# Optimization experiments

Hardware: AMD Instinct MI355X
Metric: run time of the kernel (lower is better)

Reference implementation:

```python
import jax, jax.numpy as jnp
import numpy as np

B, C, H, W = 16, 256, 56, 56
CR = C // 4
PAD = 1
NUM_ITERS = 5


def _conv(x, w, b):
    # NCHW conv, stride 1, 'same' padding for k=3
    y = jax.lax.conv_general_dilated(x, w, (1, 1), [(PAD, PAD), (PAD, PAD)],
                                     dimension_numbers=('NCHW', 'OIHW', 'NCHW'))
    return y + b[None, :, None, None]


_GAUSS = np.array([[1., 2., 1.], [2., 4., 2.], [1., 2., 1.]], np.float32) / 16.0


def _crf_rnn(unary1, compat, spatial_w):
    # Mean-field CRF-RNN refinement with num_labels=2 and a fixed spatial Gaussian kernel.
    unary = jnp.concatenate([unary1, -unary1], axis=1)  # [B,2,h,w] two-label unary from 1-ch map
    gk = jnp.tile(jnp.asarray(_GAUSS)[None, None], (2, 1, 1, 1))  # depthwise [2,1,3,3]
    q = jax.nn.softmax(unary, axis=1)
    for _ in range(NUM_ITERS):
        blur = jax.lax.conv_general_dilated(q, gk, (1, 1), [(1, 1), (1, 1)],
                                            dimension_numbers=('NCHW', 'OIHW', 'NCHW'),
                                            feature_group_count=2)
        msg = blur * spatial_w[None, :, None, None]          # filter-output weighting
        pairwise = jnp.einsum('lk,bkhw->blhw', compat, msg)  # label compatibility transform
        q = jax.nn.softmax(unary - pairwise, axis=1)
    return q[:, 1:2]  # P(label=1) as refined spatial attention map


def _forward(x, w0_0, b0_0, w0_1, b0_1, w0_2, b0_2, w0_3, b0_3, w0_4, b0_4,
             w1, b1, w2, b2, fc1_w, fc2_w, fc2_b, crf_compat, crf_spatial_w):
    f1 = jax.nn.relu(_conv(x, w0_0, b0_0))             # [B,C,H,W]  (dominant compute)
    f1c = jnp.mean(f1, axis=(2, 3), keepdims=True)      # global avg pool -> [B,C,1,1]
    f2 = jax.nn.relu(_conv(f1c, w0_1, b0_1))            # [B,C,1,1]
    v_c = jax.nn.sigmoid(f1c[:, :, 0, 0] @ fc1_w.T)[:, :, None, None]  # channel attention
    f_c = v_c * f2
    f3 = jax.nn.relu(_conv(f_c, w0_2, b0_2))
    f4 = jax.nn.relu(_conv(f3, w0_3, b0_3))
    f3s = jax.nn.relu(_conv(f3, w1, b1))                # [B,C/4,1,1]
    v0s = jax.nn.relu(_conv(f3s, w2, b2))               # [B,1,1,1] initial spatial attention
    v_s = _crf_rnn(v0s, crf_compat, crf_spatial_w)      # CRF-RNN refined attention
    f_s = v_s * f4
    f_r = jax.nn.relu(_conv(f_s, w0_4, b0_4))
    f_ra = jnp.mean(f_r, axis=(2, 3), keepdims=True)    # [B,C,1,1]
    p_n = jax.nn.sigmoid(f_ra[:, :, 0, 0] @ fc2_w.T + fc2_b)  # [B,1]
    return p_n


def setup_inputs() -> dict:
    key = jax.random.key(0)
    ks = jax.random.split(key, 16)

    def w(k, shape, fan):
        return jax.random.normal(k, shape, jnp.float32) / np.sqrt(fan)

    inp = {'x': jax.random.normal(ks[0], (B, C, H, W), jnp.float32)}
    for i in range(5):
        inp['w0_%d' % i] = w(ks[1 + i], (C, C, 3, 3), C * 9)
        inp['b0_%d' % i] = jnp.zeros((C,), jnp.float32)
    inp['w1'] = w(ks[6], (CR, C, 3, 3), C * 9)
    inp['b1'] = jnp.zeros((CR,), jnp.float32)
    inp['w2'] = w(ks[7], (1, CR, 3, 3), CR * 9)
    inp['b2'] = jnp.zeros((1,), jnp.float32)
    inp['fc1_w'] = w(ks[8], (C, C), C)
    inp['fc2_w'] = w(ks[9], (1, C), C)
    inp['fc2_b'] = jnp.zeros((1,), jnp.float32)
    inp['crf_compat'] = jnp.asarray([[0., 1.], [1., 0.]], jnp.float32) + 0.1 * jax.random.normal(ks[10], (2, 2), jnp.float32)
    inp['crf_spatial_w'] = jnp.ones((2,), jnp.float32)
    return inp


def reference(x, w0_0, b0_0, w0_1, b0_1, w0_2, b0_2, w0_3, b0_3, w0_4, b0_4,
              w1, b1, w2, b2, fc1_w, fc2_w, fc2_b, crf_compat, crf_spatial_w):
    return _forward(x, w0_0, b0_0, w0_1, b0_1, w0_2, b0_2, w0_3, b0_3, w0_4, b0_4,
                    w1, b1, w2, b2, fc1_w, fc2_w, fc2_b, crf_compat, crf_spatial_w)
```

## Files before the change

### kernel.cpp

```cpp
#include <hip/hip_runtime.h>
#include <hip/hip_bf16.h>

typedef __bf16 bf16x8 __attribute__((ext_vector_type(8)));
typedef float f32x4 __attribute__((ext_vector_type(4)));

#define NB 16
#define NC 256
#define NHW 3136
#define NW 56
#define PROW 58
#define PPLANE (58 * 58)

__device__ __forceinline__ unsigned short f2bf(float f) {
    union { float f; unsigned u; } v; v.f = f;
    unsigned r = v.u + 0x7FFFu + ((v.u >> 16) & 1u);
    return (unsigned short)(r >> 16);
}

__device__ __forceinline__ void gload_lds16(const void* g, void* l) {
    __builtin_amdgcn_global_load_lds((const __attribute__((address_space(1))) void*)g,
                                     (__attribute__((address_space(3))) void*)l, 16, 0, 0);
}

__global__ void k_zero_halo(unsigned short* __restrict__ xT) {
    int t = blockIdx.x * 256 + threadIdx.x;
    if (t >= 128 * 228) return;
    int plane = t / 228, h = t % 228;
    int row, xc;
    if (h < 58)       { row = 0;       xc = h; }
    else if (h < 116) { row = 57;      xc = h - 58; }
    else if (h < 172) { row = h - 115; xc = 0; }
    else              { row = h - 171; xc = 57; }
    size_t e = ((size_t)plane * PPLANE + (size_t)row * PROW + xc) * 32;
    uint4 z = {0u, 0u, 0u, 0u};
    *(uint4*)(xT + e)      = z;
    *(uint4*)(xT + e + 8)  = z;
    *(uint4*)(xT + e + 16) = z;
    *(uint4*)(xT + e + 24) = z;
}

__global__ void k_repack_x(const float* __restrict__ x, unsigned short* __restrict__ xT) {
    __shared__ float tile[32][33];
    int bid = blockIdx.x;
    int hwb = bid % 98;
    int cb = (bid / 98) % 8;
    int b = bid / (98 * 8);
    int tid = threadIdx.x;
    {
        int c_l = tid >> 5, hw_l = tid & 31;
        const float* src = x + ((size_t)b * NC + (size_t)cb * 32) * NHW + hwb * 32;
#pragma unroll
        for (int r = 0; r < 4; ++r) {
            int c = c_l + r * 8;
            tile[c][hw_l] = src[(size_t)c * NHW + hw_l];
        }
    }
    __syncthreads();
    {
        int qd = tid & 7, hw2 = tid >> 3;
        int hw = hwb * 32 + hw2;
        int y = hw / 56, xp = hw - y * 56;
        unsigned short* dst = xT + ((size_t)(b * 8 + cb) * PPLANE +
                                    (size_t)(y + 1) * PROW + (xp + 1)) * 32 + qd * 4;
        ushort4 v;
        v.x = f2bf(tile[qd * 4 + 0][hw2]);
        v.y = f2bf(tile[qd * 4 + 1][hw2]);
        v.z = f2bf(tile[qd * 4 + 2][hw2]);
        v.w = f2bf(tile[qd * 4 + 3][hw2]);
        *(ushort4*)dst = v;
    }
}

__global__ void k_repack_w(const float* __restrict__ w0_0, const float* __restrict__ w0_1,
                           const float* __restrict__ w0_2, const float* __restrict__ w0_3,
                           const float* __restrict__ w0_4, const float* __restrict__ w1,
                           const float* __restrict__ w2, const float* __restrict__ fc1_w,
                           unsigned short* __restrict__ Bp, float* __restrict__ w01T,
                           float* __restrict__ w02T, float* __restrict__ w03T,
                           float* __restrict__ w04T, float* __restrict__ fc1T,
                           float* __restrict__ w1T, float* __restrict__ w2c) {
    int bid = blockIdx.x, tid = threadIdx.x;
    if (bid < 2304) {
        int idx = bid * 256 + tid;
        int q = idx & 31;
        int n = (idx >> 5) & 255;
        int s = idx >> 13;
        int tap = s >> 3;
        int ic = (s & 7) * 32 + q;
        Bp[idx] = f2bf(w0_0[(size_t)n * 2304 + (size_t)ic * 9 + tap]);
        return;
    }
    int tb = bid - 2304;
    __shared__ float tile[64][65];
    if (tb < 84) {
        const float* src; float* dst;
        int sstr, estr, off, OD, o0, i0;
        if (tb < 80) {
            int arr = tb >> 4, t16 = tb & 15;
            o0 = (t16 >> 2) * 64; i0 = (t16 & 3) * 64; OD = 256;
            sstr = 2304; estr = 9; off = 4;
            switch (arr) {
                case 0: src = w0_1; dst = w01T; break;
                case 1: src = w0_2; dst = w02T; break;
                case 2: src = w0_3; dst = w03T; break;
                case 3: src = w0_4; dst = w04T; break;
                default: src = fc1_w; dst = fc1T; sstr = 256; estr = 1; off = 0; break;
            }
        } else {
            int t4i = tb - 80; o0 = 0; i0 = t4i * 64; OD = 64;
            sstr = 2304; estr = 9; off = 4;
            src = w1; dst = w1T;
        }
        int i1 = tid & 63, o4 = tid >> 6;
#pragma unroll
        for (int p = 0; p < 16; ++p) {
            int oo = p * 4 + o4;
            tile[oo][i1] = src[(size_t)(o0 + oo) * sstr + (size_t)(i0 + i1) * estr + off];
        }
        __syncthreads();
        int o1 = tid & 63, i4 = tid >> 6;
#pragma unroll
        for (int p = 0; p < 16; ++p) {
            int ii = p * 4 + i4;
            dst[(size_t)(i0 + ii) * OD + o0 + o1] = tile[o1][ii];
        }
    } else {
        if (tid < 64) w2c[tid] = w2[tid * 9 + 4];
    }
}

__global__ __launch_bounds__(256, 2) void k_conv(
    const unsigned short* __restrict__ xT,
    const unsigned short* __restrict__ Bp,
    const float* __restrict__ b0_0,
    float* __restrict__ partial) {
    __shared__ __align__(16) char alds[2][16384];
    int blk = blockIdx.x;
    int b = blk / 28, pt = blk % 28;
    int tid = threadIdx.x;
    int lane = tid & 63, wave = tid >> 6;
    int col = lane & 15, grp = lane >> 4;
    int nbase = wave * 64;

    int swz = (lane & 3) ^ ((lane >> 3) & 3);
    int pixoff = ((lane >> 2) << 6) + (swz << 4);
    const char* xbytes = (const char*)xT;
    size_t stage_row = (size_t)(pt * 2 + wave) * (PROW * 64);

    int p_[7][3];
#pragma unroll
    for (int mt = 0; mt < 7; ++mt) {
        int q = mt * 16 + col;
        int r = q >= 56 ? 1 : 0;
        int x = q - 56 * r;
#pragma unroll
        for (int dxi = 0; dxi < 3; ++dxi) {
            int ppx = x + dxi;
            int slot = grp ^ ((ppx >> 1) & 3);
            p_[mt][dxi] = r * 4096 + ppx * 64 + slot * 16;
        }
    }
    int boff[4];
#pragma unroll
    for (int nt = 0; nt < 4; ++nt)
        boff[nt] = ((nbase + nt * 16 + col) * 32 + grp * 8) * 2;

    f32x4 acc[7][4];
#pragma unroll
    for (int mt = 0; mt < 7; ++mt)
#pragma unroll
        for (int nt = 0; nt < 4; ++nt) {
            acc[mt][nt][0] = 0.f; acc[mt][nt][1] = 0.f;
            acc[mt][nt][2] = 0.f; acc[mt][nt][3] = 0.f;
        }

    {
        const char* g0 = xbytes + (size_t)(b * 8) * (PPLANE * 64) + stage_row + pixoff;
        char* l0 = &alds[0][wave * 4096];
#pragma unroll
        for (int j = 0; j < 4; ++j)
            gload_lds16(g0 + j * 1024, l0 + j * 1024);
    }
    __syncthreads();

    for (int icb = 0; icb < 8; ++icb) {
        int cur = icb & 1;
        if (icb < 7) {
            const char* g = xbytes + (size_t)(b * 8 + icb + 1) * (PPLANE * 64) + stage_row + pixoff;
            char* l = &alds[cur ^ 1][wave * 4096];
#pragma unroll
            for (int j = 0; j < 4; ++j)
                gload_lds16(g + j * 1024, l + j * 1024);
        }
        const char* abuf = alds[cur];
#pragma unroll
        for (int dy = -1; dy <= 1; ++dy) {
#pragma unroll
            for (int dx = -1; dx <= 1; ++dx) {
                int tap = (dy + 1) * 3 + (dx + 1);
                const char* bplane = (const char*)(Bp + ((size_t)(tap * 8 + icb) << 13));
                bf16x8 af[7], bfr[4];
#pragma unroll
                for (int nt = 0; nt < 4; ++nt)
                    bfr[nt] = *(const bf16x8*)(bplane + boff[nt]);
#pragma unroll
                for (int mt = 0; mt < 7; ++mt)
                    af[mt] = *(const bf16x8*)(abuf + (p_[mt][dx + 1] + (dy + 1) * 4096));
#pragma unroll
                for (int mt = 0; mt < 7; ++mt)
#pragma unroll
                    for (int nt = 0; nt < 4; ++nt)
                        acc[mt][nt] = __builtin_amdgcn_mfma_f32_16x16x32_bf16(af[mt], bfr[nt], acc[mt][nt], 0, 0, 0);
            }
        }
        __syncthreads();
    }

#pragma unroll
    for (int nt = 0; nt < 4; ++nt) {
        int n = nbase + nt * 16 + col;
        float bias = b0_0[n];
        float s = 0.f;
#pragma unroll
        for (int mt = 0; mt < 7; ++mt)
#pragma unroll
            for (int j = 0; j < 4; ++j)
                s += fmaxf(acc[mt][nt][j] + bias, 0.f);
        s += __shfl_down(s, 32);
        s += __shfl_down(s, 16);
        if (grp == 0) partial[(size_t)blk * NC + n] = s;
    }
}

__global__ __launch_bounds__(1024) void k_tail(
    const float* __restrict__ partial,
    const float* __restrict__ w01T, const float* __restrict__ fc1T,
    const float* __restrict__ w02T, const float* __restrict__ w03T,
    const float* __restrict__ w04T, const float* __restrict__ w1T,
    const float* __restrict__ w2c,
    const float* __restrict__ b0_1, const float* __restrict__ b0_2,
    const float* __restrict__ b0_3, const float* __restrict__ b0_4,
    const float* __restrict__ b1, const float* __restrict__ b2,
    const float* __restrict__ fc2_w, const float* __restrict__ fc2_b,
    const float* __restrict__ compat, const float* __restrict__ spatial_w,
    float* __restrict__ out) {
    __shared__ float fc[256], t2[256], t3[256], t4[256];
    __shared__ float rA[4][256], rB[4][256];
    __shared__ float red64[64];
    __shared__ float vs_sh;
    int b = blockIdx.x, tid = threadIdx.x;
    int o = tid & 255, seg = tid >> 8;
    int i0 = seg * 64;

    {
        float s = 0.f;
        const float* pp = partial + (size_t)b * 28 * 256 + o;
#pragma unroll
        for (int r = seg * 7; r < seg * 7 + 7; ++r) s += pp[r * 256];
        rA[seg][o] = s;
    }
    __syncthreads();
    if (seg == 0) fc[o] = (rA[0][o] + rA[1][o] + rA[2][o] + rA[3][o]) * (1.f / 3136.f);
    __syncthreads();

    {
        float a2 = 0.f, av = 0.f;
        for (int i = i0; i < i0 + 64; ++i) {
            float fi = fc[i];
            a2 = fmaf(w01T[i * 256 + o], fi, a2);
            av = fmaf(fc1T[i * 256 + o], fi, av);
        }
        rA[seg][o] = a2; rB[seg][o] = av;
    }
    __syncthreads();
    if (seg == 0) {
        float A = rA[0][o] + rA[1][o] + rA[2][o] + rA[3][o];
        float V = rB[0][o] + rB[1][o] + rB[2][o] + rB[3][o];
        t2[o] = fmaxf(A + b0_1[o], 0.f) / (1.f + expf(-V));
    }
    __syncthreads();

    {
        float a3 = 0.f;
        for (int i = i0; i < i0 + 64; ++i) a3 = fmaf(w02T[i * 256 + o], t2[i], a3);
        rA[seg][o] = a3;
    }
    __syncthreads();
    if (seg == 0) t3[o] = fmaxf(rA[0][o] + rA[1][o] + rA[2][o] + rA[3][o] + b0_2[o], 0.f);
    __syncthreads();

    {
        float a4 = 0.f;
        for (int i = i0; i < i0 + 64; ++i) a4 = fmaf(w03T[i * 256 + o], t3[i], a4);
        rA[seg][o] = a4;
        int o64 = tid & 63, s16 = tid >> 6;
        float a5 = 0.f;
        for (int i = s16 * 16; i < s16 * 16 + 16; ++i) a5 = fmaf(w1T[i * 64 + o64], t3[i], a5);
        ((float*)rB)[s16 * 64 + o64] = a5;
    }
    __syncthreads();
    if (seg == 0) t4[o] = fmaxf(rA[0][o] + rA[1][o] + rA[2][o] + rA[3][o] + b0_3[o], 0.f);
    if (tid < 64) {
        float a5 = 0.f;
        const float* rb = (const float*)rB;
#pragma unroll
        for (int j = 0; j < 16; ++j) a5 += rb[j * 64 + tid];
        float v = fmaxf(a5 + b1[tid], 0.f);
        red64[tid] = v * w2c[tid];
    }
    __syncthreads();
    if (tid == 0) {
        float u = 0.f;
        for (int i = 0; i < 64; ++i) u += red64[i];
        u = fmaxf(u + b2[0], 0.f);
        float c00 = compat[0], c01 = compat[1], c10 = compat[2], c11 = compat[3];
        float sw0 = spatial_w[0], sw1 = spatial_w[1];
        float q1 = 1.f / (1.f + expf(2.f * u));
        float q0 = 1.f - q1;
        for (int it = 0; it < 5; ++it) {
            float m0 = q0 * 0.25f * sw0;
            float m1 = q1 * 0.25f * sw1;
            float pw0 = c00 * m0 + c01 * m1;
            float pw1 = c10 * m0 + c11 * m1;
            float z0 = u - pw0, z1 = -u - pw1;
            q1 = 1.f / (1.f + expf(z0 - z1));
            q0 = 1.f - q1;
        }
        vs_sh = q1;
    }
    __syncthreads();

    {
        float a6 = 0.f;
        for (int i = i0; i < i0 + 64; ++i) a6 = fmaf(w04T[i * 256 + o], t4[i], a6);
        rA[seg][o] = a6;
    }
    __syncthreads();
    if (seg == 0) {
        float A = rA[0][o] + rA[1][o] + rA[2][o] + rA[3][o];
        float fr = fmaxf(vs_sh * A + b0_4[o], 0.f);
        rB[0][o] = fr * fc2_w[o];
    }
    __syncthreads();
    if (tid < 128) rB[0][tid] += rB[0][tid + 128];
    __syncthreads();
    if (tid < 64) rB[0][tid] += rB[0][tid + 64];
    __syncthreads();
    if (tid == 0) {
        float t = 0.f;
        for (int i = 0; i < 64; ++i) t += rB[0][i];
        out[b] = 1.f / (1.f + expf(-(t + fc2_b[0])));
    }
}

extern "C" void kernel_launch(void* const* d_in, const int* in_sizes, int n_in,
                              void* d_out, int out_size, void* d_ws, size_t ws_size,
                              hipStream_t stream) {
    const float* x     = (const float*)d_in[0];
    const float* w0_0  = (const float*)d_in[1];
    const float* b0_0  = (const float*)d_in[2];
    const float* w0_1  = (const float*)d_in[3];
    const float* b0_1  = (const float*)d_in[4];
    const float* w0_2  = (const float*)d_in[5];
    const float* b0_2  = (const float*)d_in[6];
    const float* w0_3  = (const float*)d_in[7];
    const float* b0_3  = (const float*)d_in[8];
    const float* w0_4  = (const float*)d_in[9];
    const float* b0_4  = (const float*)d_in[10];
    const float* w1    = (const float*)d_in[11];
    const float* b1    = (const float*)d_in[12];
    const float* w2    = (const float*)d_in[13];
    const float* b2    = (const float*)d_in[14];
    const float* fc1_w = (const float*)d_in[15];
    const float* fc2_w = (const float*)d_in[16];
    const float* fc2_b = (const float*)d_in[17];
    const float* compat = (const float*)d_in[18];
    const float* sw     = (const float*)d_in[19];

    unsigned short* xT = (unsigned short*)d_ws;
    unsigned short* Bp = xT + (size_t)128 * PPLANE * 32;
    float* w01T = (float*)(Bp + 589824);
    float* w02T = w01T + 65536;
    float* w03T = w02T + 65536;
    float* w04T = w03T + 65536;
    float* fc1T = w04T + 65536;
    float* w1T  = fc1T + 65536;
    float* w2c  = w1T + 16384;
    float* partial = w2c + 64;

    hipLaunchKernelGGL(k_zero_halo, dim3((128 * 228 + 255) / 256), dim3(256), 0, stream, xT);
    hipLaunchKernelGGL(k_repack_x, dim3(16 * 8 * 98), dim3(256), 0, stream, x, xT);
    hipLaunchKernelGGL(k_repack_w, dim3(2304 + 85), dim3(256), 0, stream,
                       w0_0, w0_1, w0_2, w0_3, w0_4, w1, w2, fc1_w,
                       Bp, w01T, w02T, w03T, w04T, fc1T, w1T, w2c);
    hipLaunchKernelGGL(k_conv, dim3(448), dim3(256), 0, stream, xT, Bp, b0_0, partial);
    hipLaunchKernelGGL(k_tail, dim3(16), dim3(1024), 0, stream, partial,
                       w01T, fc1T, w02T, w03T, w04T, w1T, w2c,
                       b0_1, b0_2, b0_3, b0_4, b1, b2, fc2_w, fc2_b, compat, sw,
                       (float*)d_out);
}
```

Baseline: 213.1 us.

## Merge prep kernels and retile conv to one output row per block

The halo-zero, input repack and weight repack kernels are merged into a single prep launch to cut launch overhead. The conv kernel now tiles one output row per block (896 blocks) instead of two rows (448). That means 4 M-tiles of 16 instead of 7, with 64 padded pixels and the 8 tail pixels masked out. The per-block LDS stage drops to 3 padded rows, which allows 3 blocks per CU for better occupancy and wave balance. The cost is some wasted MFMA work on the padding and more halo rows re-read per output row; the tail reduction is adjusted to 56 partials per batch.

New measurement: 244.9 us. 14.9% more time.

```diff
diff --git a/kernel.cpp b/kernel.cpp
--- a/kernel.cpp
+++ b/kernel.cpp
@@ -11,6 +11,10 @@
 #define PROW 58
 #define PPLANE (58 * 58)
 
+#define NRX 12544
+#define NRW 2389
+#define NHALO 114
+
 __device__ __forceinline__ unsigned short f2bf(float f) {
     union { float f; unsigned u; } v; v.f = f;
     unsigned r = v.u + 0x7FFFu + ((v.u >> 16) & 1u);
@@ -22,142 +26,149 @@
                                      (__attribute__((address_space(3))) void*)l, 16, 0, 0);
 }
 
-__global__ void k_zero_halo(unsigned short* __restrict__ xT) {
-    int t = blockIdx.x * 256 + threadIdx.x;
-    if (t >= 128 * 228) return;
-    int plane = t / 228, h = t % 228;
-    int row, xc;
-    if (h < 58)       { row = 0;       xc = h; }
-    else if (h < 116) { row = 57;      xc = h - 58; }
-    else if (h < 172) { row = h - 115; xc = 0; }
-    else              { row = h - 171; xc = 57; }
-    size_t e = ((size_t)plane * PPLANE + (size_t)row * PROW + xc) * 32;
-    uint4 z = {0u, 0u, 0u, 0u};
-    *(uint4*)(xT + e)      = z;
-    *(uint4*)(xT + e + 8)  = z;
-    *(uint4*)(xT + e + 16) = z;
-    *(uint4*)(xT + e + 24) = z;
-}
-
-__global__ void k_repack_x(const float* __restrict__ x, unsigned short* __restrict__ xT) {
-    __shared__ float tile[32][33];
-    int bid = blockIdx.x;
-    int hwb = bid % 98;
-    int cb = (bid / 98) % 8;
-    int b = bid / (98 * 8);
-    int tid = threadIdx.x;
-    {
-        int c_l = tid >> 5, hw_l = tid & 31;
-        const float* src = x + ((size_t)b * NC + (size_t)cb * 32) * NHW + hwb * 32;
-#pragma unroll
-        for (int r = 0; r < 4; ++r) {
-            int c = c_l + r * 8;
-            tile[c][hw_l] = src[(size_t)c * NHW + hw_l];
-        }
-    }
-    __syncthreads();
-    {
-        int qd = tid & 7, hw2 = tid >> 3;
-        int hw = hwb * 32 + hw2;
-        int y = hw / 56, xp = hw - y * 56;
-        unsigned short* dst = xT + ((size_t)(b * 8 + cb) * PPLANE +
-                                    (size_t)(y + 1) * PROW + (xp + 1)) * 32 + qd * 4;
-        ushort4 v;
-        v.x = f2bf(tile[qd * 4 + 0][hw2]);
-        v.y = f2bf(tile[qd * 4 + 1][hw2]);
-        v.z = f2bf(tile[qd * 4 + 2][hw2]);
-        v.w = f2bf(tile[qd * 4 + 3][hw2]);
-        *(ushort4*)dst = v;
-    }
-}
-
-__global__ void k_repack_w(const float* __restrict__ w0_0, const float* __restrict__ w0_1,
-                           const float* __restrict__ w0_2, const float* __restrict__ w0_3,
-                           const float* __restrict__ w0_4, const float* __restrict__ w1,
-                           const float* __restrict__ w2, const float* __restrict__ fc1_w,
-                           unsigned short* __restrict__ Bp, float* __restrict__ w01T,
-                           float* __restrict__ w02T, float* __restrict__ w03T,
-                           float* __restrict__ w04T, float* __restrict__ fc1T,
-                           float* __restrict__ w1T, float* __restrict__ w2c) {
+__global__ void k_prep(const float* __restrict__ x,
+                       const float* __restrict__ w0_0, const float* __restrict__ w0_1,
+                       const float* __restrict__ w0_2, const float* __restrict__ w0_3,
+                       const float* __restrict__ w0_4, const float* __restrict__ w1,
+                       const float* __restrict__ w2, const float* __restrict__ fc1_w,
+                       unsigned short* __restrict__ xT, unsigned short* __restrict__ Bp,
+                       float* __restrict__ w01T, float* __restrict__ w02T,
+                       float* __restrict__ w03T, float* __restrict__ w04T,
+                       float* __restrict__ fc1T, float* __restrict__ w1T,
+                       float* __restrict__ w2c) {
+    __shared__ float sh[64 * 65];
     int bid = blockIdx.x, tid = threadIdx.x;
-    if (bid < 2304) {
-        int idx = bid * 256 + tid;
-        int q = idx & 31;
-        int n = (idx >> 5) & 255;
-        int s = idx >> 13;
-        int tap = s >> 3;
-        int ic = (s & 7) * 32 + q;
-        Bp[idx] = f2bf(w0_0[(size_t)n * 2304 + (size_t)ic * 9 + tap]);
+
+    if (bid < NRX) {
+        int hwb = bid % 98;
+        int cb = (bid / 98) % 8;
+        int b = bid / (98 * 8);
+        {
+            int c_l = tid >> 5, hw_l = tid & 31;
+            const float* src = x + ((size_t)b * NC + (size_t)cb * 32) * NHW + hwb * 32;
+#pragma unroll
+            for (int r = 0; r < 4; ++r) {
+                int c = c_l + r * 8;
+                sh[c * 33 + hw_l] = src[(size_t)c * NHW + hw_l];
+            }
+        }
+        __syncthreads();
+        {
+            int qd = tid & 7, hw2 = tid >> 3;
+            int hw = hwb * 32 + hw2;
+            int y = hw / 56, xp = hw - y * 56;
+            unsigned short* dst = xT + ((size_t)(b * 8 + cb) * PPLANE +
+                                        (size_t)(y + 1) * PROW + (xp + 1)) * 32 + qd * 4;
+            ushort4 v;
+            v.x = f2bf(sh[(qd * 4 + 0) * 33 + hw2]);
+            v.y = f2bf(sh[(qd * 4 + 1) * 33 + hw2]);
+            v.z = f2bf(sh[(qd * 4 + 2) * 33 + hw2]);
+            v.w = f2bf(sh[(qd * 4 + 3) * 33 + hw2]);
+            *(ushort4*)dst = v;
+        }
         return;
     }
-    int tb = bid - 2304;
-    __shared__ float tile[64][65];
-    if (tb < 84) {
-        const float* src; float* dst;
-        int sstr, estr, off, OD, o0, i0;
-        if (tb < 80) {
-            int arr = tb >> 4, t16 = tb & 15;
-            o0 = (t16 >> 2) * 64; i0 = (t16 & 3) * 64; OD = 256;
-            sstr = 2304; estr = 9; off = 4;
-            switch (arr) {
-                case 0: src = w0_1; dst = w01T; break;
-                case 1: src = w0_2; dst = w02T; break;
-                case 2: src = w0_3; dst = w03T; break;
-                case 3: src = w0_4; dst = w04T; break;
-                default: src = fc1_w; dst = fc1T; sstr = 256; estr = 1; off = 0; break;
+    if (bid < NRX + NRW) {
+        int bw = bid - NRX;
+        if (bw < 2304) {
+            int idx = bw * 256 + tid;
+            int q = idx & 31;
+            int n = (idx >> 5) & 255;
+            int s = idx >> 13;
+            int tap = s >> 3;
+            int ic = (s & 7) * 32 + q;
+            Bp[idx] = f2bf(w0_0[(size_t)n * 2304 + (size_t)ic * 9 + tap]);
+            return;
+        }
+        int tb = bw - 2304;
+        if (tb < 84) {
+            const float* src; float* dst;
+            int sstr, estr, off, OD, o0, i0;
+            if (tb < 80) {
+                int arr = tb >> 4, t16 = tb & 15;
+                o0 = (t16 >> 2) * 64; i0 = (t16 & 3) * 64; OD = 256;
+                sstr = 2304; estr = 9; off = 4;
+                switch (arr) {
+                    case 0: src = w0_1; dst = w01T; break;
+                    case 1: src = w0_2; dst = w02T; break;
+                    case 2: src = w0_3; dst = w03T; break;
+                    case 3: src = w0_4; dst = w04T; break;
+                    default: src = fc1_w; dst = fc1T; sstr = 256; estr = 1; off = 0; break;
+                }
+            } else {
+                int t4i = tb - 80; o0 = 0; i0 = t4i * 64; OD = 64;
+                sstr = 2304; estr = 9; off = 4;
+                src = w1; dst = w1T;
+            }
+            int i1 = tid & 63, o4 = tid >> 6;
+#pragma unroll
+            for (int p = 0; p < 16; ++p) {
+                int oo = p * 4 + o4;
+                sh[oo * 65 + i1] = src[(size_t)(o0 + oo) * sstr + (size_t)(i0 + i1) * estr + off];
+            }
+            __syncthreads();
+            int o1 = tid & 63, i4 = tid >> 6;
+#pragma unroll
+            for (int p = 0; p < 16; ++p) {
+                int ii = p * 4 + i4;
+                dst[(size_t)(i0 + ii) * OD + o0 + o1] = sh[o1 * 65 + ii];
             }
         } else {
-            int t4i = tb - 80; o0 = 0; i0 = t4i * 64; OD = 64;
-            sstr = 2304; estr = 9; off = 4;
-            src = w1; dst = w1T;
-        }
-        int i1 = tid & 63, o4 = tid >> 6;
-#pragma unroll
-        for (int p = 0; p < 16; ++p) {
-            int oo = p * 4 + o4;
-            tile[oo][i1] = src[(size_t)(o0 + oo) * sstr + (size_t)(i0 + i1) * estr + off];
-        }
-        __syncthreads();
-        int o1 = tid & 63, i4 = tid >> 6;
-#pragma unroll
-        for (int p = 0; p < 16; ++p) {
-            int ii = p * 4 + i4;
-            dst[(size_t)(i0 + ii) * OD + o0 + o1] = tile[o1][ii];
-        }
-    } else {
-        if (tid < 64) w2c[tid] = w2[tid * 9 + 4];
-    }
-}
-
-__global__ __launch_bounds__(256, 2) void k_conv(
+            if (tid < 64) w2c[tid] = w2[tid * 9 + 4];
+        }
+        return;
+    }
+    {
+        int t = (bid - NRX - NRW) * 256 + tid;
+        if (t >= 128 * 228) return;
+        int plane = t / 228, h = t % 228;
+        int row, xc;
+        if (h < 58)       { row = 0;       xc = h; }
+        else if (h < 116) { row = 57;      xc = h - 58; }
+        else if (h < 172) { row = h - 115; xc = 0; }
+        else              { row = h - 171; xc = 57; }
+        size_t e = ((size_t)plane * PPLANE + (size_t)row * PROW + xc) * 32;
+        uint4 z = {0u, 0u, 0u, 0u};
+        *(uint4*)(xT + e)      = z;
+        *(uint4*)(xT + e + 8)  = z;
+        *(uint4*)(xT + e + 16) = z;
+        *(uint4*)(xT + e + 24) = z;
+    }
+}
+
+__global__ __launch_bounds__(256, 3) void k_conv(
     const unsigned short* __restrict__ xT,
     const unsigned short* __restrict__ Bp,
     const float* __restrict__ b0_0,
     float* __restrict__ partial) {
-    __shared__ __align__(16) char alds[2][16384];
+    __shared__ __align__(16) char alds[2][12288];
     int blk = blockIdx.x;
-    int b = blk / 28, pt = blk % 28;
+    int b = blk / 56, y = blk % 56;
     int tid = threadIdx.x;
     int lane = tid & 63, wave = tid >> 6;
     int col = lane & 15, grp = lane >> 4;
     int nbase = wave * 64;
 
-    int swz = (lane & 3) ^ ((lane >> 3) & 3);
-    int pixoff = ((lane >> 2) << 6) + (swz << 4);
-    const char* xbytes = (const char*)xT;
-    size_t stage_row = (size_t)(pt * 2 + wave) * (PROW * 64);
-
-    int p_[7][3];
-#pragma unroll
-    for (int mt = 0; mt < 7; ++mt) {
+    int g_off[3]; bool g_act[3];
+#pragma unroll
+    for (int r = 0; r < 3; ++r) {
+        int c = r * 256 + tid;
+        int row = c / 232, rem = c - row * 232;
+        int px = rem >> 2, part = rem & 3;
+        g_act[r] = (c < 696);
+        g_off[r] = ((y + row) * PROW + px) * 64 + ((part ^ ((px >> 1) & 3)) << 4);
+    }
+
+    int p_[4][3];
+#pragma unroll
+    for (int mt = 0; mt < 4; ++mt) {
         int q = mt * 16 + col;
-        int r = q >= 56 ? 1 : 0;
-        int x = q - 56 * r;
 #pragma unroll
         for (int dxi = 0; dxi < 3; ++dxi) {
-            int ppx = x + dxi;
+            int ppx = q + dxi;
+            if (ppx > 63) ppx = 63;
             int slot = grp ^ ((ppx >> 1) & 3);
-            p_[mt][dxi] = r * 4096 + ppx * 64 + slot * 16;
+            p_[mt][dxi] = ppx * 64 + slot * 16;
         }
     }
     int boff[4];
@@ -165,49 +176,48 @@
     for (int nt = 0; nt < 4; ++nt)
         boff[nt] = ((nbase + nt * 16 + col) * 32 + grp * 8) * 2;
 
-    f32x4 acc[7][4];
-#pragma unroll
-    for (int mt = 0; mt < 7; ++mt)
+    f32x4 acc[4][4];
+#pragma unroll
+    for (int mt = 0; mt < 4; ++mt)
 #pragma unroll
         for (int nt = 0; nt < 4; ++nt) {
             acc[mt][nt][0] = 0.f; acc[mt][nt][1] = 0.f;
             acc[mt][nt][2] = 0.f; acc[mt][nt][3] = 0.f;
         }
 
-    {
-        const char* g0 = xbytes + (size_t)(b * 8) * (PPLANE * 64) + stage_row + pixoff;
-        char* l0 = &alds[0][wave * 4096];
-#pragma unroll
-        for (int j = 0; j < 4; ++j)
-            gload_lds16(g0 + j * 1024, l0 + j * 1024);
+    const char* xbytes = (const char*)xT;
+    {
+        const char* gp = xbytes + (size_t)(b * 8) * (PPLANE * 64);
+#pragma unroll
+        for (int r = 0; r < 3; ++r)
+            if (g_act[r]) gload_lds16(gp + g_off[r], &alds[0][r * 4096 + wave * 1024]);
     }
     __syncthreads();
 
     for (int icb = 0; icb < 8; ++icb) {
         int cur = icb & 1;
         if (icb < 7) {
-            const char* g = xbytes + (size_t)(b * 8 + icb + 1) * (PPLANE * 64) + stage_row + pixoff;
-            char* l = &alds[cur ^ 1][wave * 4096];
-#pragma unroll
-            for (int j = 0; j < 4; ++j)
-                gload_lds16(g + j * 1024, l + j * 1024);
+            const char* gp = xbytes + (size_t)(b * 8 + icb + 1) * (PPLANE * 64);
+#pragma unroll
+            for (int r = 0; r < 3; ++r)
+                if (g_act[r]) gload_lds16(gp + g_off[r], &alds[cur ^ 1][r * 4096 + wave * 1024]);
         }
         const char* abuf = alds[cur];
 #pragma unroll
-        for (int dy = -1; dy <= 1; ++dy) {
-#pragma unroll
-            for (int dx = -1; dx <= 1; ++dx) {
-                int tap = (dy + 1) * 3 + (dx + 1);
+        for (int dyi = 0; dyi < 3; ++dyi) {
+#pragma unroll
+            for (int dxi = 0; dxi < 3; ++dxi) {
+                int tap = dyi * 3 + dxi;
                 const char* bplane = (const char*)(Bp + ((size_t)(tap * 8 + icb) << 13));
-                bf16x8 af[7], bfr[4];
+                bf16x8 af[4], bfr[4];
 #pragma unroll
                 for (int nt = 0; nt < 4; ++nt)
                     bfr[nt] = *(const bf16x8*)(bplane + boff[nt]);
 #pragma unroll
-                for (int mt = 0; mt < 7; ++mt)
-                    af[mt] = *(const bf16x8*)(abuf + (p_[mt][dx + 1] + (dy + 1) * 4096));
-#pragma unroll
-                for (int mt = 0; mt < 7; ++mt)
+                for (int mt = 0; mt < 4; ++mt)
+                    af[mt] = *(const bf16x8*)(abuf + (dyi * 4096 + p_[mt][dxi]));
+#pragma unroll
+                for (int mt = 0; mt < 4; ++mt)
 #pragma unroll
                     for (int nt = 0; nt < 4; ++nt)
                         acc[mt][nt] = __builtin_amdgcn_mfma_f32_16x16x32_bf16(af[mt], bfr[nt], acc[mt][nt], 0, 0, 0);
@@ -222,13 +232,15 @@
         float bias = b0_0[n];
         float s = 0.f;
 #pragma unroll
-        for (int mt = 0; mt < 7; ++mt)
-#pragma unroll
-            for (int j = 0; j < 4; ++j)
-                s += fmaxf(acc[mt][nt][j] + bias, 0.f);
+        for (int mt = 0; mt < 4; ++mt)
+#pragma unroll
+            for (int j = 0; j < 4; ++j) {
+                int m = mt * 16 + grp * 4 + j;
+                if (m < NW) s += fmaxf(acc[mt][nt][j] + bias, 0.f);
+            }
         s += __shfl_down(s, 32);
         s += __shfl_down(s, 16);
-        if (grp == 0) partial[(size_t)blk * NC + n] = s;
+        if (grp == 0) partial[((size_t)b * NW + y) * NC + n] = s;
     }
 }
 
@@ -254,9 +266,9 @@
 
     {
         float s = 0.f;
-        const float* pp = partial + (size_t)b * 28 * 256 + o;
-#pragma unroll
-        for (int r = seg * 7; r < seg * 7 + 7; ++r) s += pp[r * 256];
+        const float* pp = partial + (size_t)b * 56 * 256 + o;
+#pragma unroll
+        for (int r = seg * 14; r < seg * 14 + 14; ++r) s += pp[r * 256];
         rA[seg][o] = s;
     }
     __syncthreads();
@@ -388,12 +400,10 @@
     float* w2c  = w1T + 16384;
     float* partial = w2c + 64;
 
-    hipLaunchKernelGGL(k_zero_halo, dim3((128 * 228 + 255) / 256), dim3(256), 0, stream, xT);
-    hipLaunchKernelGGL(k_repack_x, dim3(16 * 8 * 98), dim3(256), 0, stream, x, xT);
-    hipLaunchKernelGGL(k_repack_w, dim3(2304 + 85), dim3(256), 0, stream,
-                       w0_0, w0_1, w0_2, w0_3, w0_4, w1, w2, fc1_w,
-                       Bp, w01T, w02T, w03T, w04T, fc1T, w1T, w2c);
-    hipLaunchKernelGGL(k_conv, dim3(448), dim3(256), 0, stream, xT, Bp, b0_0, partial);
+    hipLaunchKernelGGL(k_prep, dim3(NRX + NRW + NHALO), dim3(256), 0, stream,
+                       x, w0_0, w0_1, w0_2, w0_3, w0_4, w1, w2, fc1_w,
+                       xT, Bp, w01T, w02T, w03T, w04T, fc1T, w1T, w2c);
+    hipLaunchKernelGGL(k_conv, dim3(896), dim3(256), 0, stream, xT, Bp, b0_0, partial);
     hipLaunchKernelGGL(k_tail, dim3(16), dim3(1024), 0, stream, partial,
                        w01T, fc1T, w02T, w03T, w04T, w1T, w2c,
                        b0_1, b0_2, b0_3, b0_4, b1, b2, fc2_w, fc2_b, compat, sw,
```

## Merge prep kernels, prefetch conv weight fragments, and remap conv block order

Applied to the files above, without the earlier changes.

Fuses the halo-zeroing, input repack and weight repack kernels into one launch, with each block handling more work (8 channel blocks or 8 weight chunks per block). This removes two kernel launches and their serialization. In the conv kernel, the B-operand fragments for the next tap are loaded into registers while the MFMAs for the current tap run, hiding global-load latency. The block index is also permuted across batches, presumably to spread work or cache traffic across XCDs. The prefetch adds register pressure under launch_bounds(256,2).

Result: faster. 201.8 us (-5.3%).

```diff
diff --git a/kernel.cpp b/kernel.cpp
--- a/kernel.cpp
+++ b/kernel.cpp
@@ -11,6 +11,11 @@
 #define PROW 58
 #define PPLANE (58 * 58)
 
+#define NRX2 1568
+#define NBP 288
+#define NMAT 85
+#define NHALO 114
+
 __device__ __forceinline__ unsigned short f2bf(float f) {
     union { float f; unsigned u; } v; v.f = f;
     unsigned r = v.u + 0x7FFFu + ((v.u >> 16) & 1u);
@@ -22,110 +27,114 @@
                                      (__attribute__((address_space(3))) void*)l, 16, 0, 0);
 }
 
-__global__ void k_zero_halo(unsigned short* __restrict__ xT) {
-    int t = blockIdx.x * 256 + threadIdx.x;
-    if (t >= 128 * 228) return;
-    int plane = t / 228, h = t % 228;
-    int row, xc;
-    if (h < 58)       { row = 0;       xc = h; }
-    else if (h < 116) { row = 57;      xc = h - 58; }
-    else if (h < 172) { row = h - 115; xc = 0; }
-    else              { row = h - 171; xc = 57; }
-    size_t e = ((size_t)plane * PPLANE + (size_t)row * PROW + xc) * 32;
-    uint4 z = {0u, 0u, 0u, 0u};
-    *(uint4*)(xT + e)      = z;
-    *(uint4*)(xT + e + 8)  = z;
-    *(uint4*)(xT + e + 16) = z;
-    *(uint4*)(xT + e + 24) = z;
-}
-
-__global__ void k_repack_x(const float* __restrict__ x, unsigned short* __restrict__ xT) {
-    __shared__ float tile[32][33];
-    int bid = blockIdx.x;
-    int hwb = bid % 98;
-    int cb = (bid / 98) % 8;
-    int b = bid / (98 * 8);
-    int tid = threadIdx.x;
-    {
+__global__ void k_prep(const float* __restrict__ x,
+                       const float* __restrict__ w0_0, const float* __restrict__ w0_1,
+                       const float* __restrict__ w0_2, const float* __restrict__ w0_3,
+                       const float* __restrict__ w0_4, const float* __restrict__ w1,
+                       const float* __restrict__ w2, const float* __restrict__ fc1_w,
+                       unsigned short* __restrict__ xT, unsigned short* __restrict__ Bp,
+                       float* __restrict__ w01T, float* __restrict__ w02T,
+                       float* __restrict__ w03T, float* __restrict__ w04T,
+                       float* __restrict__ fc1T, float* __restrict__ w1T,
+                       float* __restrict__ w2c) {
+    __shared__ float sh[64 * 65];
+    int bid = blockIdx.x, tid = threadIdx.x;
+
+    if (bid < NRX2) {
+        int hwb = bid % 98;
+        int b = bid / 98;
         int c_l = tid >> 5, hw_l = tid & 31;
-        const float* src = x + ((size_t)b * NC + (size_t)cb * 32) * NHW + hwb * 32;
-#pragma unroll
-        for (int r = 0; r < 4; ++r) {
-            int c = c_l + r * 8;
-            tile[c][hw_l] = src[(size_t)c * NHW + hw_l];
-        }
-    }
-    __syncthreads();
-    {
         int qd = tid & 7, hw2 = tid >> 3;
         int hw = hwb * 32 + hw2;
         int y = hw / 56, xp = hw - y * 56;
-        unsigned short* dst = xT + ((size_t)(b * 8 + cb) * PPLANE +
-                                    (size_t)(y + 1) * PROW + (xp + 1)) * 32 + qd * 4;
-        ushort4 v;
-        v.x = f2bf(tile[qd * 4 + 0][hw2]);
-        v.y = f2bf(tile[qd * 4 + 1][hw2]);
-        v.z = f2bf(tile[qd * 4 + 2][hw2]);
-        v.w = f2bf(tile[qd * 4 + 3][hw2]);
-        *(ushort4*)dst = v;
-    }
-}
-
-__global__ void k_repack_w(const float* __restrict__ w0_0, const float* __restrict__ w0_1,
-                           const float* __restrict__ w0_2, const float* __restrict__ w0_3,
-                           const float* __restrict__ w0_4, const float* __restrict__ w1,
-                           const float* __restrict__ w2, const float* __restrict__ fc1_w,
-                           unsigned short* __restrict__ Bp, float* __restrict__ w01T,
-                           float* __restrict__ w02T, float* __restrict__ w03T,
-                           float* __restrict__ w04T, float* __restrict__ fc1T,
-                           float* __restrict__ w1T, float* __restrict__ w2c) {
-    int bid = blockIdx.x, tid = threadIdx.x;
-    if (bid < 2304) {
-        int idx = bid * 256 + tid;
-        int q = idx & 31;
-        int n = (idx >> 5) & 255;
-        int s = idx >> 13;
-        int tap = s >> 3;
-        int ic = (s & 7) * 32 + q;
-        Bp[idx] = f2bf(w0_0[(size_t)n * 2304 + (size_t)ic * 9 + tap]);
+        for (int cb = 0; cb < 8; ++cb) {
+            const float* src = x + ((size_t)b * NC + (size_t)cb * 32) * NHW + hwb * 32;
+#pragma unroll
+            for (int r = 0; r < 4; ++r) {
+                int c = c_l + r * 8;
+                sh[c * 33 + hw_l] = src[(size_t)c * NHW + hw_l];
+            }
+            __syncthreads();
+            unsigned short* dst = xT + ((size_t)(b * 8 + cb) * PPLANE +
+                                        (size_t)(y + 1) * PROW + (xp + 1)) * 32 + qd * 4;
+            ushort4 v;
+            v.x = f2bf(sh[(qd * 4 + 0) * 33 + hw2]);
+            v.y = f2bf(sh[(qd * 4 + 1) * 33 + hw2]);
+            v.z = f2bf(sh[(qd * 4 + 2) * 33 + hw2]);
+            v.w = f2bf(sh[(qd * 4 + 3) * 33 + hw2]);
+            *(ushort4*)dst = v;
+            __syncthreads();
+        }
         return;
     }
-    int tb = bid - 2304;
-    __shared__ float tile[64][65];
-    if (tb < 84) {
-        const float* src; float* dst;
-        int sstr, estr, off, OD, o0, i0;
-        if (tb < 80) {
-            int arr = tb >> 4, t16 = tb & 15;
-            o0 = (t16 >> 2) * 64; i0 = (t16 & 3) * 64; OD = 256;
-            sstr = 2304; estr = 9; off = 4;
-            switch (arr) {
-                case 0: src = w0_1; dst = w01T; break;
-                case 1: src = w0_2; dst = w02T; break;
-                case 2: src = w0_3; dst = w03T; break;
-                case 3: src = w0_4; dst = w04T; break;
-                default: src = fc1_w; dst = fc1T; sstr = 256; estr = 1; off = 0; break;
+    if (bid < NRX2 + NBP) {
+        int bw = bid - NRX2;
+#pragma unroll
+        for (int k = 0; k < 8; ++k) {
+            int idx = (bw * 8 + k) * 256 + tid;
+            int q = idx & 31;
+            int n = (idx >> 5) & 255;
+            int s = idx >> 13;
+            int tap = s >> 3;
+            int ic = (s & 7) * 32 + q;
+            Bp[idx] = f2bf(w0_0[(size_t)n * 2304 + (size_t)ic * 9 + tap]);
+        }
+        return;
+    }
+    if (bid < NRX2 + NBP + NMAT) {
+        int tb = bid - NRX2 - NBP;
+        if (tb < 84) {
+            const float* src; float* dst;
+            int sstr, estr, off, OD, o0, i0;
+            if (tb < 80) {
+                int arr = tb >> 4, t16 = tb & 15;
+                o0 = (t16 >> 2) * 64; i0 = (t16 & 3) * 64; OD = 256;
+                sstr = 2304; estr = 9; off = 4;
+                switch (arr) {
+                    case 0: src = w0_1; dst = w01T; break;
+                    case 1: src = w0_2; dst = w02T; break;
+                    case 2: src = w0_3; dst = w03T; break;
+                    case 3: src = w0_4; dst = w04T; break;
+                    default: src = fc1_w; dst = fc1T; sstr = 256; estr = 1; off = 0; break;
+                }
+            } else {
+                int t4i = tb - 80; o0 = 0; i0 = t4i * 64; OD = 64;
+                sstr = 2304; estr = 9; off = 4;
+                src = w1; dst = w1T;
+            }
+            int i1 = tid & 63, o4 = tid >> 6;
+#pragma unroll
+            for (int p = 0; p < 16; ++p) {
+                int oo = p * 4 + o4;
+                sh[oo * 65 + i1] = src[(size_t)(o0 + oo) * sstr + (size_t)(i0 + i1) * estr + off];
+            }
+            __syncthreads();
+            int o1 = tid & 63, i4 = tid >> 6;
+#pragma unroll
+            for (int p = 0; p < 16; ++p) {
+                int ii = p * 4 + i4;
+                dst[(size_t)(i0 + ii) * OD + o0 + o1] = sh[o1 * 65 + ii];
             }
         } else {
-            int t4i = tb - 80; o0 = 0; i0 = t4i * 64; OD = 64;
-            sstr = 2304; estr = 9; off = 4;
-            src = w1; dst = w1T;
-        }
-        int i1 = tid & 63, o4 = tid >> 6;
-#pragma unroll
-        for (int p = 0; p < 16; ++p) {
-            int oo = p * 4 + o4;
-            tile[oo][i1] = src[(size_t)(o0 + oo) * sstr + (size_t)(i0 + i1) * estr + off];
-        }
-        __syncthreads();
-        int o1 = tid & 63, i4 = tid >> 6;
-#pragma unroll
-        for (int p = 0; p < 16; ++p) {
-            int ii = p * 4 + i4;
-            dst[(size_t)(i0 + ii) * OD + o0 + o1] = tile[o1][ii];
-        }
-    } else {
-        if (tid < 64) w2c[tid] = w2[tid * 9 + 4];
+            if (tid < 64) w2c[tid] = w2[tid * 9 + 4];
+        }
+        return;
+    }
+    {
+        int t = (bid - NRX2 - NBP - NMAT) * 256 + tid;
+        if (t >= 128 * 228) return;
+        int plane = t / 228, h = t % 228;
+        int row, xc;
+        if (h < 58)       { row = 0;       xc = h; }
+        else if (h < 116) { row = 57;      xc = h - 58; }
+        else if (h < 172) { row = h - 115; xc = 0; }
+        else              { row = h - 171; xc = 57; }
+        size_t e = ((size_t)plane * PPLANE + (size_t)row * PROW + xc) * 32;
+        uint4 z = {0u, 0u, 0u, 0u};
+        *(uint4*)(xT + e)      = z;
+        *(uint4*)(xT + e + 8)  = z;
+        *(uint4*)(xT + e + 16) = z;
+        *(uint4*)(xT + e + 24) = z;
     }
 }
 
@@ -135,8 +144,8 @@
     const float* __restrict__ b0_0,
     float* __restrict__ partial) {
     __shared__ __align__(16) char alds[2][16384];
-    int blk = blockIdx.x;
-    int b = blk / 28, pt = blk % 28;
+    int lblk = ((blockIdx.x & 7) * 56) + (blockIdx.x >> 3);
+    int b = lblk / 28, pt = lblk % 28;
     int tid = threadIdx.x;
     int lane = tid & 63, wave = tid >> 6;
     int col = lane & 15, grp = lane >> 4;
@@ -180,6 +189,13 @@
 #pragma unroll
         for (int j = 0; j < 4; ++j)
             gload_lds16(g0 + j * 1024, l0 + j * 1024);
+    }
+    bf16x8 bcur[4], bnxt[4];
+    {
+        const char* bp0 = (const char*)Bp;
+#pragma unroll
+        for (int nt = 0; nt < 4; ++nt)
+            bcur[nt] = *(const bf16x8*)(bp0 + boff[nt]);
     }
     __syncthreads();
 
@@ -194,24 +210,27 @@
         }
         const char* abuf = alds[cur];
 #pragma unroll
-        for (int dy = -1; dy <= 1; ++dy) {
-#pragma unroll
-            for (int dx = -1; dx <= 1; ++dx) {
-                int tap = (dy + 1) * 3 + (dx + 1);
-                const char* bplane = (const char*)(Bp + ((size_t)(tap * 8 + icb) << 13));
-                bf16x8 af[7], bfr[4];
+        for (int tap = 0; tap < 9; ++tap) {
+            int nicb = (tap == 8) ? icb + 1 : icb;
+            int ntap = (tap == 8) ? 0 : tap + 1;
+            if (nicb < 8) {
+                const char* bp = (const char*)Bp + ((size_t)(ntap * 8 + nicb) << 13);
 #pragma unroll
                 for (int nt = 0; nt < 4; ++nt)
-                    bfr[nt] = *(const bf16x8*)(bplane + boff[nt]);
-#pragma unroll
-                for (int mt = 0; mt < 7; ++mt)
-                    af[mt] = *(const bf16x8*)(abuf + (p_[mt][dx + 1] + (dy + 1) * 4096));
-#pragma unroll
-                for (int mt = 0; mt < 7; ++mt)
-#pragma unroll
-                    for (int nt = 0; nt < 4; ++nt)
-                        acc[mt][nt] = __builtin_amdgcn_mfma_f32_16x16x32_bf16(af[mt], bfr[nt], acc[mt][nt], 0, 0, 0);
+                    bnxt[nt] = *(const bf16x8*)(bp + boff[nt]);
             }
+            int dyi = tap / 3, dxi = tap % 3;
+            bf16x8 af[7];
+#pragma unroll
+            for (int mt = 0; mt < 7; ++mt)
+                af[mt] = *(const bf16x8*)(abuf + (p_[mt][dxi] + dyi * 4096));
+#pragma unroll
+            for (int mt = 0; mt < 7; ++mt)
+#pragma unroll
+                for (int nt = 0; nt < 4; ++nt)
+                    acc[mt][nt] = __builtin_amdgcn_mfma_f32_16x16x32_bf16(af[mt], bcur[nt], acc[mt][nt], 0, 0, 0);
+#pragma unroll
+            for (int nt = 0; nt < 4; ++nt) bcur[nt] = bnxt[nt];
         }
         __syncthreads();
     }
@@ -228,7 +247,7 @@
                 s += fmaxf(acc[mt][nt][j] + bias, 0.f);
         s += __shfl_down(s, 32);
         s += __shfl_down(s, 16);
-        if (grp == 0) partial[(size_t)blk * NC + n] = s;
+        if (grp == 0) partial[(size_t)lblk * NC + n] = s;
     }
 }
 
@@ -388,11 +407,9 @@
     float* w2c  = w1T + 16384;
     float* partial = w2c + 64;
 
-    hipLaunchKernelGGL(k_zero_halo, dim3((128 * 228 + 255) / 256), dim3(256), 0, stream, xT);
-    hipLaunchKernelGGL(k_repack_x, dim3(16 * 8 * 98), dim3(256), 0, stream, x, xT);
-    hipLaunchKernelGGL(k_repack_w, dim3(2304 + 85), dim3(256), 0, stream,
-                       w0_0, w0_1, w0_2, w0_3, w0_4, w1, w2, fc1_w,
-                       Bp, w01T, w02T, w03T, w04T, fc1T, w1T, w2c);
+    hipLaunchKernelGGL(k_prep, dim3(NRX2 + NBP + NMAT + NHALO), dim3(256), 0, stream,
+                       x, w0_0, w0_1, w0_2, w0_3, w0_4, w1, w2, fc1_w,
+                       xT, Bp, w01T, w02T, w03T, w04T, fc1T, w1T, w2c);
     hipLaunchKernelGGL(k_conv, dim3(448), dim3(256), 0, stream, xT, Bp, b0_0, partial);
     hipLaunchKernelGGL(k_tail, dim3(16), dim3(1024), 0, stream, partial,
                        w01T, fc1T, w02T, w03T, w04T, w1T, w2c,
```
